# Optimization experiments

Measured on AMD Instinct MI355X. Metric: run time of the kernel, lower is better.

The kernel has to match this reference:

```python
import jax, jax.numpy as jnp
import numpy as np

L, B, S, H, NH, DH, I, MAXP, NL = 4, 8, 512, 1024, 32, 32, 4096, 512, 20
EPS = 1e-12


def setup_inputs() -> dict:
    key = jax.random.key(0)
    ks = jax.random.split(key, 12)
    sc = 0.02
    w = lambda k, shape: jax.random.normal(k, shape, jnp.float32) * sc
    p = {}
    p['hidden_states'] = jax.random.normal(ks[0], (B, S, H), jnp.float32)
    p['attention_mask'] = jnp.ones((B, S), jnp.float32)
    p['Wq'] = w(ks[1], (L, H, H)); p['bq'] = jnp.zeros((L, H), jnp.float32)
    p['Wk'] = w(ks[2], (L, H, H)); p['bk'] = jnp.zeros((L, H), jnp.float32)
    p['Wv'] = w(ks[3], (L, H, H)); p['bv'] = jnp.zeros((L, H), jnp.float32)
    p['Wo'] = w(ks[4], (L, H, H)); p['bo'] = jnp.zeros((L, H), jnp.float32)
    p['ln1_g'] = jnp.ones((L, H), jnp.float32); p['ln1_b'] = jnp.zeros((L, H), jnp.float32)
    p['W1'] = w(ks[5], (L, H, I)); p['b1'] = jnp.zeros((L, I), jnp.float32)
    p['W2'] = w(ks[6], (L, I, H)); p['b2'] = jnp.zeros((L, H), jnp.float32)
    p['ln2_g'] = jnp.ones((L, H), jnp.float32); p['ln2_b'] = jnp.zeros((L, H), jnp.float32)
    p['rel_emb'] = w(ks[7], (L, 2 * MAXP - 1, DH))
    p['pool_W'] = w(ks[8], (3 * H, H)); p['pool_b'] = jnp.zeros((H,), jnp.float32)
    p['pool_ln_g'] = jnp.ones((H,), jnp.float32); p['pool_ln_b'] = jnp.zeros((H,), jnp.float32)
    p['cls_W'] = w(ks[9], (H, NL)); p['cls_b'] = jnp.zeros((NL,), jnp.float32)
    return p


def _ln(x, g, b):
    mu = jnp.mean(x, -1, keepdims=True)
    var = jnp.mean(jnp.square(x - mu), -1, keepdims=True)
    return (x - mu) * jax.lax.rsqrt(var + EPS) * g + b


def reference(hidden_states, attention_mask, Wq, bq, Wk, bk, Wv, bv, Wo, bo,
              ln1_g, ln1_b, W1, b1, W2, b2, ln2_g, ln2_b, rel_emb,
              pool_W, pool_b, pool_ln_g, pool_ln_b, cls_W, cls_b):
    b, s, h = hidden_states.shape
    # extended additive attention mask (0 -> -1e9)
    mask_add = (1.0 - attention_mask)[:, None, None, :] * -1e9
    pos = jnp.arange(s)
    rel_idx = pos[:, None] - pos[None, :] + MAXP - 1  # [s, s] in [0, 2*MAXP-2]
    x = hidden_states
    for l in range(L):
        heads = lambda t: t.reshape(b, s, NH, DH).transpose(0, 2, 1, 3)
        q = heads(x @ Wq[l] + bq[l])
        k = heads(x @ Wk[l] + bk[l])
        v = heads(x @ Wv[l] + bv[l])
        # learned relative-position bias; note head_size == num_heads by construction
        rel = rel_emb[l][rel_idx].transpose(2, 0, 1)  # [DH==NH, s, s]
        scores = jnp.einsum('bhqd,bhkd->bhqk', q, k) + rel[None]
        scores = scores / np.float32(np.sqrt(DH)) + mask_add
        probs = jax.nn.softmax(scores, axis=-1)
        ctx = jnp.einsum('bhqk,bhkd->bhqd', probs, v).transpose(0, 2, 1, 3).reshape(b, s, h)
        x = _ln(ctx @ Wo[l] + bo[l] + x, ln1_g[l], ln1_b[l])
        inner = jax.nn.gelu(x @ W1[l] + b1[l], approximate=False) @ W2[l] + b2[l]
        x = _ln(x + inner, ln2_g[l], ln2_b[l])
    # AdvancedPooling: mean + max + first token
    m = attention_mask[..., None]
    mean_pool = jnp.sum(x * m, axis=1) / jnp.sum(attention_mask, axis=1, keepdims=True)
    max_pool = jnp.max(x + (1.0 - m) * -1e9, axis=1)
    pooled = jnp.concatenate([mean_pool, max_pool, x[:, 0]], axis=-1)
    pooled = _ln(pooled @ pool_W + pool_b, pool_ln_g, pool_ln_b)
    return pooled @ cls_W + cls_b
```

## Files before the change

kernel.cpp:

```cpp
#include <hip/hip_runtime.h>
#include <math.h>

typedef __attribute__((ext_vector_type(8))) _Float16 f16x8;
typedef __attribute__((ext_vector_type(4))) float f32x4;

__device__ __forceinline__ ushort f2h(float x) {
  union { _Float16 h; ushort u; } c;
  c.h = (_Float16)x;
  return c.u;
}
__device__ __forceinline__ void gl_lds16(const ushort* g, ushort* l) {
  __builtin_amdgcn_global_load_lds(
      (const __attribute__((address_space(1))) unsigned int*)g,
      (__attribute__((address_space(3))) unsigned int*)l, 16, 0, 0);
}
__device__ __forceinline__ f32x4 mfma16(f16x8 a, f16x8 b, f32x4 c) {
  return __builtin_amdgcn_mfma_f32_16x16x32_f16(a, b, c, 0, 0, 0);
}

__device__ __forceinline__ float block_reduce_sum(float v, float* sb) {
#pragma unroll
  for (int o = 32; o > 0; o >>= 1) v += __shfl_down(v, o, 64);
  const int t = threadIdx.x;
  if ((t & 63) == 0) sb[t >> 6] = v;
  __syncthreads();
  v = sb[0] + sb[1] + sb[2] + sb[3];
  __syncthreads();
  return v;
}

__global__ __launch_bounds__(256) void acast(const float* __restrict__ X,
                                             ushort* __restrict__ H, int n4) {
  const int i = blockIdx.x * 256 + threadIdx.x;
  if (i >= n4) return;
  const float4 x = ((const float4*)X)[i];
  ushort4 h;
  h.x = f2h(x.x); h.y = f2h(x.y); h.z = f2h(x.z); h.w = f2h(x.w);
  ((ushort4*)H)[i] = h;
}

__global__ __launch_bounds__(256) void concat3(const float* __restrict__ a,
                                               const float* __restrict__ b,
                                               const float* __restrict__ c,
                                               float* __restrict__ o) {
  const int i = blockIdx.x * 256 + threadIdx.x;
  o[i] = i < 1024 ? a[i] : (i < 2048 ? b[i - 1024] : c[i - 2048]);
}

__global__ __launch_bounds__(256) void wcast_t(const float* __restrict__ W,
                                               ushort* __restrict__ T,
                                               int K, int N) {
  __shared__ float s[32][33];
  const int tx = threadIdx.x & 31, ty = threadIdx.x >> 5;
  const int n0 = blockIdx.x * 32, k0 = blockIdx.y * 32;
#pragma unroll
  for (int i = 0; i < 4; ++i)
    s[ty + i * 8][tx] = W[(size_t)(k0 + ty + i * 8) * N + n0 + tx];
  __syncthreads();
#pragma unroll
  for (int i = 0; i < 4; ++i) {
    const int n = ty + i * 8;
    T[(size_t)(n0 + n) * K + k0 + tx] = f2h(s[tx][n]);
  }
}

__global__ __launch_bounds__(256) void wcast_t3(const float* __restrict__ W0,
                                                const float* __restrict__ W1,
                                                const float* __restrict__ W2,
                                                ushort* __restrict__ T) {
  __shared__ float s[32][33];
  const float* W = blockIdx.z == 0 ? W0 : (blockIdx.z == 1 ? W1 : W2);
  ushort* Tp = T + (size_t)blockIdx.z * 1024 * 1024;
  const int tx = threadIdx.x & 31, ty = threadIdx.x >> 5;
  const int n0 = blockIdx.x * 32, k0 = blockIdx.y * 32;
#pragma unroll
  for (int i = 0; i < 4; ++i)
    s[ty + i * 8][tx] = W[(size_t)(k0 + ty + i * 8) * 1024 + n0 + tx];
  __syncthreads();
#pragma unroll
  for (int i = 0; i < 4; ++i) {
    const int n = ty + i * 8;
    Tp[(size_t)(n0 + n) * 1024 + k0 + tx] = f2h(s[tx][n]);
  }
}

template <int EPI>
__global__ __launch_bounds__(512, 2) void gemm256(
    const ushort* __restrict__ A, const ushort* __restrict__ B,
    const float* __restrict__ bias, float* __restrict__ C,
    ushort* __restrict__ O, int M, int N, int K) {
  __shared__ __align__(16) ushort sA[2][8192], sB[2][8192];
  const int t = threadIdx.x, w = t >> 6, lane = t & 63;
  const int llo = lane & 15, lhi = lane >> 4;
  const int wm = w >> 2, wn = w & 3;
  const int rb = w >> 2, ko = w & 3;

  const int gx = gridDim.x;
  int wg = blockIdx.y * gx + blockIdx.x;
  const int nwg = gx * gridDim.y;
  wg = (wg & 7) * (nwg >> 3) + (wg >> 3);
  const int bm = (wg / gx) * 256, bn = (wg % gx) * 256;

  const ushort* pA0 = A + (size_t)(bm + rb * 128 + lane) * K + ko * 8;
  const ushort* pA1 = pA0 + (size_t)64 * K;
  const ushort* pB0 = B + (size_t)(bn + rb * 128 + lane) * K + ko * 8;
  const ushort* pB1 = pB0 + (size_t)64 * K;

  auto STAGE = [&](int buf, int k0) {
    gl_lds16(pA0 + k0, &sA[buf][ko * 2048 + rb * 1024]);
    gl_lds16(pA1 + k0, &sA[buf][ko * 2048 + rb * 1024 + 512]);
    gl_lds16(pB0 + k0, &sB[buf][ko * 2048 + rb * 1024]);
    gl_lds16(pB1 + k0, &sB[buf][ko * 2048 + rb * 1024 + 512]);
  };

  f32x4 acc[8][4] = {};
  const int NT = K >> 5;
  STAGE(0, 0);
  __syncthreads();
  int cur = 0;
  for (int kt = 0; kt < NT; ++kt) {
    if (kt + 1 < NT) STAGE(cur ^ 1, (kt + 1) << 5);
    f16x8 a[8], bfr[4];
#pragma unroll
    for (int f = 0; f < 8; ++f)
      a[f] = *(const f16x8*)&sA[cur][lhi * 2048 + (wm * 128 + f * 16 + llo) * 8];
#pragma unroll
    for (int f = 0; f < 4; ++f)
      bfr[f] = *(const f16x8*)&sB[cur][lhi * 2048 + (wn * 64 + f * 16 + llo) * 8];
#pragma unroll
    for (int fm = 0; fm < 8; ++fm)
#pragma unroll
      for (int fn = 0; fn < 4; ++fn)
        acc[fm][fn] = mfma16(a[fm], bfr[fn], acc[fm][fn]);
    __syncthreads();
    cur ^= 1;
  }

#pragma unroll
  for (int fm = 0; fm < 8; ++fm) {
    const int row0 = bm + wm * 128 + fm * 16 + lhi * 4;
#pragma unroll
    for (int fn = 0; fn < 4; ++fn) {
      const int col = bn + wn * 64 + fn * 16 + llo;
      const float bc = bias[col];
      if (EPI == 5) {
        if (col < 2048) {
          const size_t base = (size_t)(col >> 10) * (4096 * 1024) + (col & 1023);
#pragma unroll
          for (int r = 0; r < 4; ++r)
            O[base + (size_t)(row0 + r) * 1024] = f2h(acc[fm][fn][r] + bc);
        } else {
          const int c = col - 2048;
          ushort4 vh;
#pragma unroll
          for (int r = 0; r < 4; ++r) ((ushort*)&vh)[r] = f2h(acc[fm][fn][r] + bc);
          const size_t o = (size_t)8 * 1024 * 1024 +
              ((size_t)(((row0 >> 9) * 32 + (c >> 5)) * 32 + (c & 31))) * 512 +
              (row0 & 511);
          *(ushort4*)(O + o) = vh;
        }
      } else {
#pragma unroll
        for (int r = 0; r < 4; ++r) {
          const size_t o = (size_t)(row0 + r) * N + col;
          float v = acc[fm][fn][r] + bc;
          v = 0.5f * v * (1.f + erff(v * 0.70710678118654752f));
          O[o] = f2h(v);
        }
      }
    }
  }
}

template <int EPI, int KSPLIT>
__global__ __launch_bounds__(256, 2) void gemm_mfma(
    const ushort* __restrict__ A, const ushort* __restrict__ B,
    const float* __restrict__ bias, const float* __restrict__ res,
    float* __restrict__ C, float* __restrict__ C2, ushort* __restrict__ O,
    int M, int N, int K) {
  __shared__ __align__(16) ushort sA[2][4096], sB[2][4096];
  const int t = threadIdx.x, w = t >> 6, lane = t & 63;
  const int llo = lane & 15, lhi = lane >> 4;
  const int wm = w >> 1, wn = w & 1;
  const int z = (KSPLIT > 1) ? blockIdx.z : 0;
  const int Ks = K / KSPLIT;

  const int gx = gridDim.x;
  int wg = blockIdx.y * gx + blockIdx.x;
  const int nwg = gx * gridDim.y;
  wg = (wg & 7) * (nwg >> 3) + (wg >> 3);
  const int bm = (wg / gx) * 128, bn = (wg % gx) * 128;

  const ushort* pA0 = A + (size_t)(bm + lane) * K + w * 8 + z * Ks;
  const ushort* pA1 = pA0 + (size_t)64 * K;
  const ushort* pB0 = B + (size_t)(bn + lane) * K + w * 8 + z * Ks;
  const ushort* pB1 = pB0 + (size_t)64 * K;

  auto STAGE = [&](int buf, int k0) {
    gl_lds16(pA0 + k0, &sA[buf][w * 1024]);
    gl_lds16(pA1 + k0, &sA[buf][w * 1024 + 512]);
    gl_lds16(pB0 + k0, &sB[buf][w * 1024]);
    gl_lds16(pB1 + k0, &sB[buf][w * 1024 + 512]);
  };

  f32x4 acc[4][4] = {};
  const int NT = Ks >> 5;
  STAGE(0, 0);
  __syncthreads();
  int cur = 0;
  for (int kt = 0; kt < NT; ++kt) {
    if (kt + 1 < NT) STAGE(cur ^ 1, (kt + 1) << 5);
    f16x8 a[4], bfr[4];
#pragma unroll
    for (int f = 0; f < 4; ++f) {
      a[f] = *(const f16x8*)&sA[cur][lhi * 1024 + (wm * 64 + f * 16 + llo) * 8];
      bfr[f] = *(const f16x8*)&sB[cur][lhi * 1024 + (wn * 64 + f * 16 + llo) * 8];
    }
#pragma unroll
    for (int fm = 0; fm < 4; ++fm)
#pragma unroll
      for (int fn = 0; fn < 4; ++fn)
        acc[fm][fn] = mfma16(a[fm], bfr[fn], acc[fm][fn]);
    __syncthreads();
    cur ^= 1;
  }

#pragma unroll
  for (int fm = 0; fm < 4; ++fm) {
    const int row0 = bm + wm * 64 + fm * 16 + lhi * 4;
#pragma unroll
    for (int fn = 0; fn < 4; ++fn) {
      const int col = bn + wn * 64 + fn * 16 + llo;
      const float bc = bias[col];
#pragma unroll
      for (int r = 0; r < 4; ++r) {
        const size_t o = (size_t)(row0 + r) * N + col;
        if (KSPLIT == 1 || z == 0)
          C[o] = acc[fm][fn][r] + bc + res[o];
        else
          C2[o] = acc[fm][fn][r];
      }
    }
  }
}

__global__ __launch_bounds__(512, 2) void attn_mfma(
    const ushort* __restrict__ Qg, const ushort* __restrict__ Kg,
    const ushort* __restrict__ Vg, const float* __restrict__ mask,
    const float* __restrict__ rel_l, ushort* __restrict__ Cg) {
  __shared__ __align__(16) ushort sK[16384], sV[16384];
  __shared__ __align__(16) ushort sP[5120];
  __shared__ float rel_s[1024];
  __shared__ float madd[512];

  const int h = blockIdx.x, b = blockIdx.y, z = blockIdx.z;
  const int t = threadIdx.x, w = t >> 6, lane = t & 63;
  const int llo = lane & 15, lhi = lane >> 4;
  const float SCALE = 0.17677669529663687f;

#pragma unroll
  for (int it = 0; it < 4; ++it) {
    const int task = t + it * 512;
    const int s = task >> 2, oct = task & 3;
    const size_t g = (size_t)(b * 512 + s) * 1024 + h * 32 + oct * 8;
    *(uint4*)&sK[oct * 4096 + s * 8] = *(const uint4*)(Kg + g);
  }
#pragma unroll
  for (int it = 0; it < 4; ++it) {
    const int task = t + it * 512;
    const int d = task >> 6, ko = task & 63;
    const size_t g = (size_t)((b * 32 + h) * 32 + d) * 512 + ko * 8;
    *(uint4*)&sV[ko * 256 + d * 8] = *(const uint4*)(Vg + g);
  }
  for (int i = t; i < 1023; i += 512) rel_s[i] = rel_l[(size_t)i * 32 + h];
  for (int i = t; i < 512; i += 512) madd[i] = (1.f - mask[b * 512 + i]) * -1e9f;
  __syncthreads();

  uint* wP = (uint*)(sP + w * 640 + llo * 40);
  const ushort* rP = sP + w * 640 + llo * 40;

  for (int qt = 0; qt < 2; ++qt) {
    const int q = z * 256 + w * 32 + qt * 16 + llo;
    const size_t qg = (size_t)(b * 512 + q) * 1024 + h * 32 + lhi * 8;
    const f16x8 fQ = *(const f16x8*)(Qg + qg);
    float m = -INFINITY, l = 0.f;
    f32x4 acc0 = {0.f, 0.f, 0.f, 0.f};
    f32x4 acc1 = {0.f, 0.f, 0.f, 0.f};

    for (int kt2 = 0; kt2 < 16; ++kt2) {
      float p[8];
      float tm = -INFINITY;
#pragma unroll
      for (int sub = 0; sub < 2; ++sub) {
        const int kt = kt2 * 2 + sub;
        const f16x8 fK = *(const f16x8*)&sK[lhi * 4096 + (kt * 16 + llo) * 8];
        f32x4 s4 = {0.f, 0.f, 0.f, 0.f};
        s4 = mfma16(fK, fQ, s4);
#pragma unroll
        for (int r = 0; r < 4; ++r) {
          const int k = kt * 16 + lhi * 4 + r;
          const float sv = (s4[r] + rel_s[q - k + 511]) * SCALE + madd[k];
          p[sub * 4 + r] = sv;
          tm = fmaxf(tm, sv);
        }
      }
      tm = fmaxf(tm, __shfl_xor(tm, 16));
      tm = fmaxf(tm, __shfl_xor(tm, 32));
      const float nm = fmaxf(m, tm);
      const float sc = __expf(m - nm);
      float ts = 0.f;
#pragma unroll
      for (int i = 0; i < 8; ++i) {
        p[i] = __expf(p[i] - nm);
        ts += p[i];
      }
      ts += __shfl_xor(ts, 16);
      ts += __shfl_xor(ts, 32);
      l = l * sc + ts;
      m = nm;
      acc0 *= sc;
      acc1 *= sc;
#pragma unroll
      for (int sub = 0; sub < 2; ++sub) {
        wP[sub * 8 + lhi * 2 + 0] =
            (uint)f2h(p[sub * 4 + 0]) | ((uint)f2h(p[sub * 4 + 1]) << 16);
        wP[sub * 8 + lhi * 2 + 1] =
            (uint)f2h(p[sub * 4 + 2]) | ((uint)f2h(p[sub * 4 + 3]) << 16);
      }
      const f16x8 fP = *(const f16x8*)(rP + lhi * 8);
      const int vb = (kt2 * 4 + lhi) * 256;
      const f16x8 fV0 = *(const f16x8*)&sV[vb + llo * 8];
      const f16x8 fV1 = *(const f16x8*)&sV[vb + (16 + llo) * 8];
      acc0 = mfma16(fV0, fP, acc0);
      acc1 = mfma16(fV1, fP, acc1);
    }

    const float invl = 1.f / l;
    const size_t ob = (size_t)(b * 512 + q) * 1024 + h * 32;
    ushort4 oh;
#pragma unroll
    for (int r = 0; r < 4; ++r) ((ushort*)&oh)[r] = f2h(acc0[r] * invl);
    *(ushort4*)(Cg + ob + lhi * 4) = oh;
#pragma unroll
    for (int r = 0; r < 4; ++r) ((ushort*)&oh)[r] = f2h(acc1[r] * invl);
    *(ushort4*)(Cg + ob + 16 + lhi * 4) = oh;
  }
}

__global__ __launch_bounds__(256) void ln_kernel(
    const float* __restrict__ X, const float* __restrict__ X2,
    const float* __restrict__ g, const float* __restrict__ bt,
    float* __restrict__ out, ushort* __restrict__ O) {
  __shared__ float sb[4];
  const int row = blockIdx.x, t = threadIdx.x;
  float4 x = *(const float4*)&X[(size_t)row * 1024 + t * 4];
  if (X2) {
    const float4 y = *(const float4*)&X2[(size_t)row * 1024 + t * 4];
    x.x += y.x; x.y += y.y; x.z += y.z; x.w += y.w;
  }
  const float s = block_reduce_sum(x.x + x.y + x.z + x.w, sb);
  const float mu = s * (1.f / 1024.f);
  const float dx = x.x - mu, dy = x.y - mu, dz = x.z - mu, dw = x.w - mu;
  const float ss = block_reduce_sum(dx * dx + dy * dy + dz * dz + dw * dw, sb);
  const float rs = rsqrtf(ss * (1.f / 1024.f) + 1e-12f);
  const float4 gv = *(const float4*)&g[t * 4];
  const float4 bv = *(const float4*)&bt[t * 4];
  float4 o;
  o.x = dx * rs * gv.x + bv.x;
  o.y = dy * rs * gv.y + bv.y;
  o.z = dz * rs * gv.z + bv.z;
  o.w = dw * rs * gv.w + bv.w;
  *(float4*)&out[(size_t)row * 1024 + t * 4] = o;
  if (O) {
    ushort4 vh;
    vh.x = f2h(o.x); vh.y = f2h(o.y); vh.z = f2h(o.z); vh.w = f2h(o.w);
    *(ushort4*)&O[(size_t)row * 1024 + t * 4] = vh;
  }
}

__global__ __launch_bounds__(128) void pool_part(
    const float* __restrict__ X, const float* __restrict__ mask,
    float* __restrict__ psum, float* __restrict__ pmax,
    float* __restrict__ pcnt) {
  const int cb = blockIdx.x, b = blockIdx.y, sb = blockIdx.z;
  const int col = cb * 128 + threadIdx.x;
  float sum = 0.f, mx = -INFINITY, cnt = 0.f;
  for (int i = 0; i < 128; ++i) {
    const int s = sb * 128 + i;
    const float v = X[(size_t)(b * 512 + s) * 1024 + col];
    const float mk = mask[b * 512 + s];
    sum = fmaf(v, mk, sum);
    cnt += mk;
    mx = fmaxf(mx, v + (1.f - mk) * -1e9f);
  }
  psum[(size_t)(sb * 8 + b) * 1024 + col] = sum;
  pmax[(size_t)(sb * 8 + b) * 1024 + col] = mx;
  if (cb == 0 && threadIdx.x == 0) pcnt[sb * 8 + b] = cnt;
}

__global__ __launch_bounds__(256) void pool_fin(
    const float* __restrict__ X, const float* __restrict__ psum,
    const float* __restrict__ pmax, const float* __restrict__ pcnt,
    float* __restrict__ pooled) {
  const int idx = blockIdx.x * 256 + threadIdx.x;
  const int b = idx >> 10, col = idx & 1023;
  float s = 0.f, m = -INFINITY, c = 0.f;
#pragma unroll
  for (int sb = 0; sb < 4; ++sb) {
    s += psum[(size_t)(sb * 8 + b) * 1024 + col];
    m = fmaxf(m, pmax[(size_t)(sb * 8 + b) * 1024 + col]);
    c += pcnt[sb * 8 + b];
  }
  pooled[(size_t)b * 3072 + col] = s / c;
  pooled[(size_t)b * 3072 + 1024 + col] = m;
  pooled[(size_t)b * 3072 + 2048 + col] = X[(size_t)(b * 512) * 1024 + col];
}

__global__ __launch_bounds__(256) void pgemm_part(
    const float* __restrict__ P, const float* __restrict__ W,
    float* __restrict__ part) {
  __shared__ float sP[8][192];
  __shared__ float sacc[256][9];
  const int nb = blockIdx.x, kb = blockIdx.y;
  const int t = threadIdx.x;
  const int k0 = kb * 192, n0 = nb * 64;
  for (int i = t; i < 1536; i += 256)
    sP[i / 192][i % 192] = P[(size_t)(i / 192) * 3072 + k0 + i % 192];
  __syncthreads();
  const int n = t & 63, kq = t >> 6;
  float acc[8] = {};
  for (int kk = 0; kk < 48; ++kk) {
    const int k = kq * 48 + kk;
    const float wv = W[(size_t)(k0 + k) * 1024 + n0 + n];
#pragma unroll
    for (int b = 0; b < 8; ++b) acc[b] = fmaf(sP[b][k], wv, acc[b]);
  }
#pragma unroll
  for (int b = 0; b < 8; ++b) sacc[t][b] = acc[b];
  __syncthreads();
  for (int p = t; p < 512; p += 256) {
    const int b = p >> 6, nn = p & 63;
    const float v = sacc[nn][b] + sacc[64 + nn][b] + sacc[128 + nn][b] +
                    sacc[192 + nn][b];
    part[((size_t)kb * 8 + b) * 1024 + n0 + nn] = v;
  }
}

__global__ __launch_bounds__(256) void pgemm_fin(
    const float* __restrict__ part, const float* __restrict__ bias,
    float* __restrict__ out) {
  const int idx = blockIdx.x * 256 + threadIdx.x;
  const int b = idx >> 10, n = idx & 1023;
  float v = bias[n];
#pragma unroll
  for (int kb = 0; kb < 16; ++kb) v += part[((size_t)kb * 8 + b) * 1024 + n];
  out[(size_t)b * 1024 + n] = v;
}

__global__ __launch_bounds__(64) void cls_kernel(
    const float* __restrict__ X, const float* __restrict__ W,
    const float* __restrict__ bias, float* __restrict__ out) {
  const int n = blockIdx.x, b = blockIdx.y, lane = threadIdx.x;
  float a = 0.f;
#pragma unroll
  for (int i = 0; i < 16; ++i) {
    const int k = lane + i * 64;
    a = fmaf(X[(size_t)b * 1024 + k], W[(size_t)k * 20 + n], a);
  }
#pragma unroll
  for (int o = 32; o > 0; o >>= 1) a += __shfl_down(a, o, 64);
  if (lane == 0) out[b * 20 + n] = a + bias[n];
}

extern "C" void kernel_launch(void* const* d_in, const int* in_sizes, int n_in,
                              void* d_out, int out_size, void* d_ws, size_t ws_size,
                              hipStream_t stream) {
  const float* hs    = (const float*)d_in[0];
  const float* amask = (const float*)d_in[1];
  const float* Wq    = (const float*)d_in[2];
  const float* bq    = (const float*)d_in[3];
  const float* Wk    = (const float*)d_in[4];
  const float* bk    = (const float*)d_in[5];
  const float* Wv    = (const float*)d_in[6];
  const float* bv    = (const float*)d_in[7];
  const float* Wo    = (const float*)d_in[8];
  const float* bo    = (const float*)d_in[9];
  const float* ln1g  = (const float*)d_in[10];
  const float* ln1b  = (const float*)d_in[11];
  const float* W1    = (const float*)d_in[12];
  const float* b1    = (const float*)d_in[13];
  const float* W2    = (const float*)d_in[14];
  const float* b2    = (const float*)d_in[15];
  const float* ln2g  = (const float*)d_in[16];
  const float* ln2b  = (const float*)d_in[17];
  const float* rel   = (const float*)d_in[18];
  const float* poolW = (const float*)d_in[19];
  const float* poolb = (const float*)d_in[20];
  const float* plng  = (const float*)d_in[21];
  const float* plnb  = (const float*)d_in[22];
  const float* clsW  = (const float*)d_in[23];
  const float* clsb  = (const float*)d_in[24];

  char* W = (char*)d_ws;
  const size_t MB = (size_t)1 << 20;
  const size_t QK = (size_t)4096 * 1024;
  float* buf_t  = (float*)(W + 0 * MB);
  float* buf_t2 = (float*)(W + 16 * MB);
  float* buf_h1 = (float*)(W + 32 * MB);
  float* buf_x  = (float*)(W + 48 * MB);
  ushort* PL  = (ushort*)(W + 64 * MB);
  ushort* CTX = (ushort*)(W + 88 * MB);
  ushort* Xp  = CTX;
  ushort* H1  = (ushort*)(W + 96 * MB);
  ushort* F1  = (ushort*)(W + 104 * MB);
  ushort* Wt  = (ushort*)(W + 136 * MB);
  float* bcat = (float*)(W + 142 * MB);
  float* sm   = (float*)(W + 143 * MB);
  float* pooled  = sm;
  float* pool_h  = pooled + 8 * 3072;
  float* pool_h2 = pool_h + 8 * 1024;
  float* pcnt    = pool_h2 + 8 * 1024;
  float* psum    = pcnt + 64;
  float* pmax    = psum + 4 * 8 * 1024;
  float* pgpart  = pmax + 4 * 8 * 1024;

  const int n4act = (4096 * 1024) / 4;
  const dim3 gQKV(3072 / 256, 4096 / 256);
  const dim3 gF1(4096 / 256, 4096 / 256);
  const dim3 gKS(1024 / 128, 32, 2);
  const dim3 wsQ3(32, 32, 3);

  acast<<<n4act / 256, 256, 0, stream>>>(hs, Xp, n4act);

  const float* x_in = hs;
  for (int l = 0; l < 4; ++l) {
    const float* Wq_l = Wq + (size_t)l * 1024 * 1024;
    const float* Wk_l = Wk + (size_t)l * 1024 * 1024;
    const float* Wv_l = Wv + (size_t)l * 1024 * 1024;
    const float* Wo_l = Wo + (size_t)l * 1024 * 1024;
    const float* W1_l = W1 + (size_t)l * 1024 * 4096;
    const float* W2_l = W2 + (size_t)l * 4096 * 1024;

    concat3<<<12, 256, 0, stream>>>(bq + l * 1024, bk + l * 1024, bv + l * 1024, bcat);
    wcast_t3<<<wsQ3, 256, 0, stream>>>(Wq_l, Wk_l, Wv_l, Wt);
    gemm256<5><<<gQKV, 512, 0, stream>>>(Xp, Wt, bcat, nullptr, PL,
                                         4096, 3072, 1024);

    attn_mfma<<<dim3(32, 8, 2), 512, 0, stream>>>(
        PL, PL + QK, PL + 2 * QK, amask, rel + (size_t)l * 1023 * 32, CTX);

    wcast_t<<<dim3(32, 32), 256, 0, stream>>>(Wo_l, Wt, 1024, 1024);
    gemm_mfma<2, 2><<<gKS, 256, 0, stream>>>(CTX, Wt, bo + l * 1024, x_in,
                                             buf_t, buf_t2, nullptr, 4096, 1024, 1024);
    ln_kernel<<<4096, 256, 0, stream>>>(buf_t, buf_t2, ln1g + l * 1024,
                                        ln1b + l * 1024, buf_h1, H1);

    wcast_t<<<dim3(4096 / 32, 1024 / 32), 256, 0, stream>>>(W1_l, Wt, 1024, 4096);
    gemm256<1><<<gF1, 512, 0, stream>>>(H1, Wt, b1 + l * 4096, nullptr, F1,
                                        4096, 4096, 1024);
    wcast_t<<<dim3(1024 / 32, 4096 / 32), 256, 0, stream>>>(W2_l, Wt, 4096, 1024);
    gemm_mfma<2, 2><<<gKS, 256, 0, stream>>>(F1, Wt, b2 + l * 1024, buf_h1,
                                             buf_t, buf_t2, nullptr, 4096, 1024, 4096);
    ln_kernel<<<4096, 256, 0, stream>>>(buf_t, buf_t2, ln2g + l * 1024,
                                        ln2b + l * 1024, buf_x, Xp);
    x_in = buf_x;
  }

  pool_part<<<dim3(8, 8, 4), 128, 0, stream>>>(buf_x, amask, psum, pmax, pcnt);
  pool_fin<<<32, 256, 0, stream>>>(buf_x, psum, pmax, pcnt, pooled);
  pgemm_part<<<dim3(16, 16), 256, 0, stream>>>(pooled, poolW, pgpart);
  pgemm_fin<<<32, 256, 0, stream>>>(pgpart, poolb, pool_h);
  ln_kernel<<<8, 256, 0, stream>>>(pool_h, nullptr, plng, plnb, pool_h2, nullptr);
  cls_kernel<<<dim3(20, 8), 64, 0, stream>>>(pool_h2, clsW, clsb, (float*)d_out);
}
```

Measured before the change: 1.351 ms.

## Deepen GEMM K-tile to 64 with prefetch-two-ahead pipeline and vmcnt waits

The 256x256 GEMM kernel now stages 64-wide K tiles instead of 32, doubling LDS buffers, and issues loads for tile kt+2 while computing tile kt. Fine-grained s_waitcnt vmcnt plus raw s_barrier replace __syncthreads, so global-to-LDS loads can stay in flight across iterations. The aim is to hide global memory latency and halve barrier count per K. The cost is 128KB of LDS per block, which may reduce occupancy below the launch bound of 2 blocks per CU. Correctness also depends on hand-counted vmcnt values.

```diff
diff --git a/kernel.cpp b/kernel.cpp
--- a/kernel.cpp
+++ b/kernel.cpp
@@ -89,11 +89,10 @@
     const ushort* __restrict__ A, const ushort* __restrict__ B,
     const float* __restrict__ bias, float* __restrict__ C,
     ushort* __restrict__ O, int M, int N, int K) {
-  __shared__ __align__(16) ushort sA[2][8192], sB[2][8192];
+  __shared__ __align__(16) ushort sA[2][16384], sB[2][16384];
   const int t = threadIdx.x, w = t >> 6, lane = t & 63;
   const int llo = lane & 15, lhi = lane >> 4;
   const int wm = w >> 2, wn = w & 3;
-  const int rb = w >> 2, ko = w & 3;
 
   const int gx = gridDim.x;
   int wg = blockIdx.y * gx + blockIdx.x;
@@ -101,38 +100,61 @@
   wg = (wg & 7) * (nwg >> 3) + (wg >> 3);
   const int bm = (wg / gx) * 256, bn = (wg % gx) * 256;
 
-  const ushort* pA0 = A + (size_t)(bm + rb * 128 + lane) * K + ko * 8;
-  const ushort* pA1 = pA0 + (size_t)64 * K;
-  const ushort* pB0 = B + (size_t)(bn + rb * 128 + lane) * K + ko * 8;
-  const ushort* pB1 = pB0 + (size_t)64 * K;
-
-  auto STAGE = [&](int buf, int k0) {
-    gl_lds16(pA0 + k0, &sA[buf][ko * 2048 + rb * 1024]);
-    gl_lds16(pA1 + k0, &sA[buf][ko * 2048 + rb * 1024 + 512]);
-    gl_lds16(pB0 + k0, &sB[buf][ko * 2048 + rb * 1024]);
-    gl_lds16(pB1 + k0, &sB[buf][ko * 2048 + rb * 1024 + 512]);
+  const ushort* Ab = A + (size_t)(bm + lane) * K;
+  const ushort* Bb = B + (size_t)(bn + lane) * K;
+  const size_t K64 = (size_t)64 * K, K128 = (size_t)128 * K;
+
+  auto STAGE_TILE = [&](int buf, int kb) {
+#pragma unroll
+    for (int i = 0; i < 2; ++i) {
+      const int idx = i * 8 + w;
+      const int ko = idx >> 1;
+      const int rb = (idx & 1) << 6;
+      const size_t go = (idx & 1) ? K64 : 0;
+      const int lo = ko * 1024 + rb * 8;
+      gl_lds16(Ab + go + kb + ko * 8, &sA[buf][lo]);
+      gl_lds16(Ab + K128 + go + kb + ko * 8, &sA[buf][8192 + lo]);
+      gl_lds16(Bb + go + kb + ko * 8, &sB[buf][lo]);
+      gl_lds16(Bb + K128 + go + kb + ko * 8, &sB[buf][8192 + lo]);
+    }
   };
 
   f32x4 acc[8][4] = {};
-  const int NT = K >> 5;
-  STAGE(0, 0);
-  __syncthreads();
+  const int NT = K >> 6;
+  STAGE_TILE(0, 0);
+  STAGE_TILE(1, 64);
+  asm volatile("s_waitcnt vmcnt(8)" ::: "memory");
+  asm volatile("s_barrier" ::: "memory");
+
+  const int aoff = wm * 8192 + lhi * 1024;
+  const int boff = (wn >> 1) * 8192 + lhi * 1024 + ((wn & 1) * 64 + llo) * 8;
   int cur = 0;
   for (int kt = 0; kt < NT; ++kt) {
-    if (kt + 1 < NT) STAGE(cur ^ 1, (kt + 1) << 5);
-    f16x8 a[8], bfr[4];
-#pragma unroll
-    for (int f = 0; f < 8; ++f)
-      a[f] = *(const f16x8*)&sA[cur][lhi * 2048 + (wm * 128 + f * 16 + llo) * 8];
-#pragma unroll
-    for (int f = 0; f < 4; ++f)
-      bfr[f] = *(const f16x8*)&sB[cur][lhi * 2048 + (wn * 64 + f * 16 + llo) * 8];
-#pragma unroll
-    for (int fm = 0; fm < 8; ++fm)
-#pragma unroll
-      for (int fn = 0; fn < 4; ++fn)
-        acc[fm][fn] = mfma16(a[fm], bfr[fn], acc[fm][fn]);
-    __syncthreads();
+    f16x8 af[8], bf4[4];
+#pragma unroll
+    for (int kk = 0; kk < 2; ++kk) {
+      const int kof = kk * 4096;
+#pragma unroll
+      for (int f = 0; f < 8; ++f)
+        af[f] = *(const f16x8*)&sA[cur][aoff + kof + (f * 16 + llo) * 8];
+#pragma unroll
+      for (int f = 0; f < 4; ++f)
+        bf4[f] = *(const f16x8*)&sB[cur][boff + kof + f * 128];
+#pragma unroll
+      for (int fm = 0; fm < 8; ++fm)
+#pragma unroll
+        for (int fn = 0; fn < 4; ++fn)
+          acc[fm][fn] = mfma16(af[fm], bf4[fn], acc[fm][fn]);
+    }
+    asm volatile("s_barrier" ::: "memory");
+    if (kt + 2 < NT) STAGE_TILE(cur, (kt + 2) << 6);
+    if (kt + 1 < NT) {
+      if (kt + 2 < NT)
+        asm volatile("s_waitcnt vmcnt(8)" ::: "memory");
+      else
+        asm volatile("s_waitcnt vmcnt(0)" ::: "memory");
+      asm volatile("s_barrier" ::: "memory");
+    }
     cur ^= 1;
   }
 
```

Measured after the change: 1.340 ms. Within noise of the previous version (-0.8%).
